# Optimization experiments

Measured on AMD Instinct MI355X. Metric: run time of the kernel, lower is better.

## Reference

```python
import jax, jax.numpy as jnp
import numpy as np

B, NWORD, HID = 4, 24, 512


def setup_inputs() -> dict:
    key = jax.random.key(0)
    ks = jax.random.split(key, 7)
    H = HID
    scale_in = 1.0 / np.sqrt(H)
    return {
        "seqt": jax.random.normal(ks[0], (B, NWORD, 2 * H), dtype=jnp.float32),
        # ins_input_linearity: Linear(H -> 5H) with bias
        "Wi": jax.random.normal(ks[1], (5 * H, H), dtype=jnp.float32) * scale_in,
        "bi": jnp.zeros((5 * H,), dtype=jnp.float32),
        # ins_state_linearity: Linear(H -> 5H) with bias (bias init: forget slots = 1)
        "Ws": jax.random.normal(ks[2], (5 * H, H), dtype=jnp.float32) * scale_in,
        "bs": jnp.zeros((5 * H,), dtype=jnp.float32).at[H:2 * H].set(1.0),
        # ins_bilinearity: BilinearSimilarity(2H, 2H) -> scalar x^T W y
        "Wbil": jax.random.normal(ks[3], (2 * H, 2 * H), dtype=jnp.float32) * (1.0 / (2.0 * H)),
    }


def reference(seqt, Wi, bi, Ws, bs, Wbil):
    """Inside pass (do_inside) of DioLstm in training mode (soft_sum over splits).

    Chart cell (left, L) covers words [left, left+L]. Returns root v = concat(h, c).
    """
    Bn, n, twoH = seqt.shape
    H = twoH // 2
    # ins_bias buffer: ones on the two forget-gate slots [H:3H]
    ins_bias = jnp.zeros((5 * H,), dtype=seqt.dtype).at[H:3 * H].set(1.0)

    def single(seq):  # seq: [n, 2H]
        chartH = jnp.zeros((n, n, H), seq.dtype).at[:, 0].set(seq[:, :H])
        chartC = jnp.zeros((n, n, H), seq.dtype).at[:, 0].set(seq[:, H:])
        chartS = jnp.zeros((n, n), seq.dtype)  # leaf scores are 0
        for L in range(1, n):  # span length - 1 (static unroll over diagonals)
            P = n - L  # number of spans on this diagonal
            lefts = jnp.arange(P)[:, None]          # [P,1]
            ksplit = jnp.arange(L)[None, :]          # [1,L]
            # left child: (left, k); right child: (left+k+1, L-1-k)
            lH = chartH[lefts, ksplit]; lC = chartC[lefts, ksplit]; lS = chartS[lefts, ksplit]
            ridx = lefts + ksplit + 1
            rlen = jnp.broadcast_to(L - 1 - ksplit, ridx.shape)
            rH = chartH[ridx, rlen]; rC = chartC[ridx, rlen]; rS = chartS[ridx, rlen]
            lv = jnp.concatenate([lH, lC], axis=-1)  # [P,L,2H]
            rv = jnp.concatenate([rH, rC], axis=-1)
            # bilinear compatibility + child scores
            compat = jnp.einsum('pki,ij,pkj->pk', lv, Wbil, rv) + lS + rS  # [P,L]
            # projected_input + projected_state (sum once; gate slices of the sum)
            proj = (lH @ Wi.T + bi + ins_bias) + (rH @ Ws.T + bs)  # [P,L,5H]
            ig, lf, rf, g, og = jnp.split(proj, 5, axis=-1)
            ig = jax.nn.sigmoid(ig); lf = jax.nn.sigmoid(lf); rf = jax.nn.sigmoid(rf)
            g = jnp.tanh(g); og = jax.nn.sigmoid(og)
            mem = lf * lC + rf * rC + ig * g
            h = og * jnp.tanh(mem)  # [P,L,H]
            # soft_sum: torch.tensor(s_set) detaches scores -> stop_gradient on weights
            sw = jax.lax.stop_gradient(compat)
            w = jax.nn.softmax(sw, axis=-1)  # [P,L]
            Hnew = jnp.einsum('pk,pkh->ph', w, h)
            Cnew = jnp.einsum('pk,pkh->ph', w, mem)
            Snew = jnp.sum(w * sw, axis=-1)
            pidx = jnp.arange(P)
            chartH = chartH.at[pidx, L].set(Hnew)
            chartC = chartC.at[pidx, L].set(Cnew)
            chartS = chartS.at[pidx, L].set(Snew)
        # root cell v = concat(h, c)
        return jnp.concatenate([chartH[0, n - 1], chartC[0, n - 1]], axis=0)

    return jax.vmap(single)(seqt)  # [B, 2H]
```

## Files before the change

kernel.cpp:

```cpp
#include <hip/hip_runtime.h>
#include <math.h>

#define NB 4
#define NW 24
#define H 512
#define H2 1024
#define H5 2560
#define NCELL 300
#define NEED_BYTES ((size_t)72<<20)

static float* g_buf = nullptr;
__attribute__((constructor)) static void dio_alloc_ws(){
  (void)hipMalloc((void**)&g_buf, NEED_BYTES);
}

typedef __attribute__((ext_vector_type(8))) short bf16x8;
typedef __attribute__((ext_vector_type(4))) float f32x4;
typedef unsigned short ushort_t;

__device__ __forceinline__ int coff(int l){ return l*NW - (l*(l-1))/2; }
__device__ __forceinline__ float sigm(float x){ return 1.f/(1.f+__expf(-x)); }
__device__ __forceinline__ float ftanh(float x){ return 1.f - 2.f/(__expf(2.f*x)+1.f); }

__device__ __forceinline__ ushort_t f2b(float x){
  unsigned int u = __float_as_uint(x);
  u += 0x7FFF + ((u>>16)&1);
  return (ushort_t)(u>>16);
}
__device__ __forceinline__ float b2f(ushort_t h){
  return __uint_as_float(((unsigned int)h)<<16);
}
__device__ __forceinline__ void split_store(ushort_t* __restrict__ ph,
                                            ushort_t* __restrict__ pl,
                                            size_t idx, float x){
  ushort_t h = f2b(x);
  ph[idx] = h;
  pl[idx] = f2b(x - b2f(h));
}

__global__ void k_init(const float* __restrict__ seqt,
                       const float* __restrict__ Wi, const float* __restrict__ Ws,
                       const float* __restrict__ Wbil,
                       ushort_t* __restrict__ WiBh, ushort_t* __restrict__ WiBl,
                       ushort_t* __restrict__ WsBh, ushort_t* __restrict__ WsBl,
                       ushort_t* __restrict__ WbilTh, ushort_t* __restrict__ WbilTl,
                       float* __restrict__ cH, float* __restrict__ cC, float* __restrict__ cS,
                       ushort_t* __restrict__ cHbh, ushort_t* __restrict__ cHbl,
                       ushort_t* __restrict__ cCbh, ushort_t* __restrict__ cCbl){
  const int blk = blockIdx.x, t = threadIdx.x;
  if (blk < 10240){
    int i = blk*256 + t;
    const int n = H5*H;
    if (i < n) split_store(WiBh, WiBl, i, Wi[i]);
    else       split_store(WsBh, WsBl, i-n, Ws[i-n]);
  } else if (blk < 11264){
    __shared__ float tile[32][33];
    int tb = blk - 10240;
    int tr = (tb>>5)*32, tc = (tb&31)*32;
    int tx = t & 31, ty = t >> 5;
    #pragma unroll
    for (int i=0;i<32;i+=8)
      tile[ty+i][tx] = Wbil[(size_t)(tr+ty+i)*H2 + tc+tx];
    __syncthreads();
    #pragma unroll
    for (int i=0;i<32;i+=8)
      split_store(WbilTh, WbilTl, (size_t)(tc+ty+i)*H2 + tr+tx, tile[tx][ty+i]);
  } else {
    int tid = (blk-11264)*256 + t;
    if (tid < NB*NW*H){
      int b = tid/(NW*H); int r = tid%(NW*H); int i = r/H; int d = r%H;
      size_t idx = (size_t)(b*NCELL + i)*H + d;
      float hv = seqt[(size_t)(b*NW+i)*H2 + d];
      float cv = seqt[(size_t)(b*NW+i)*H2 + H + d];
      cH[idx]=hv; cC[idx]=cv;
      split_store(cHbh,cHbl,idx,hv);
      split_store(cCbh,cCbl,idx,cv);
      if (d==0) cS[b*NCELL+i] = 0.f;
    }
  }
}

__device__ __forceinline__ void mfma3(f32x4& acc, bf16x8 ah, bf16x8 al,
                                      bf16x8 bh, bf16x8 bl){
  acc = __builtin_amdgcn_mfma_f32_16x16x32_bf16(ah, bh, acc, 0,0,0);
  acc = __builtin_amdgcn_mfma_f32_16x16x32_bf16(ah, bl, acc, 0,0,0);
  acc = __builtin_amdgcn_mfma_f32_16x16x32_bf16(al, bh, acc, 0,0,0);
}

__global__ void __launch_bounds__(256)
k_projN(const ushort_t* __restrict__ WiBh, const ushort_t* __restrict__ WiBl,
        const ushort_t* __restrict__ WsBh, const ushort_t* __restrict__ WsBl,
        const ushort_t* __restrict__ WbilTh, const ushort_t* __restrict__ WbilTl,
        const float* __restrict__ bi, const float* __restrict__ bs,
        const ushort_t* __restrict__ cHbh, const ushort_t* __restrict__ cHbl,
        const ushort_t* __restrict__ cCbh, const ushort_t* __restrict__ cCbl,
        float* __restrict__ cPI, float* __restrict__ cPS, float* __restrict__ cU,
        int d, int P)
{
  __shared__ f32x4 red[4][64];
  const int t = threadIdx.x, wave = t>>6, lane = t&63;
  const int jt = blockIdx.x;
  const int m0 = blockIdx.y*16;
  const int Mtot = NB*P;
  const int nm = min(16, Mtot-m0);

  int kind, j0;
  if (jt < 160){ kind=0; j0 = jt*16; }
  else if (jt < 320){ kind=1; j0 = (jt-160)*16; }
  else { kind=2; j0 = (jt-320)*16; }

  const int r = lane & 15;
  const int q = lane >> 4;

  int mg = m0 + (r < nm ? r : 0);
  const size_t arow = (size_t)((mg/P)*NCELL + coff(d) + mg%P)*H;

  f32x4 acc = {0.f,0.f,0.f,0.f};

  if (kind < 2){
    const ushort_t* bh_ = (kind==0 ? WiBh : WsBh) + (size_t)(j0+r)*H;
    const ushort_t* bl_ = (kind==0 ? WiBl : WsBl) + (size_t)(j0+r)*H;
    const int ks = wave*128 + q*8;
    bf16x8 fah[4], fal[4], fbh[4], fbl[4];
    #pragma unroll
    for (int s=0;s<4;s++){
      const int ko = ks + s*32;
      fah[s] = *(const bf16x8*)(cHbh + arow + ko);
      fal[s] = *(const bf16x8*)(cHbl + arow + ko);
      fbh[s] = *(const bf16x8*)(bh_ + ko);
      fbl[s] = *(const bf16x8*)(bl_ + ko);
    }
    #pragma unroll
    for (int s=0;s<4;s++) mfma3(acc, fah[s], fal[s], fbh[s], fbl[s]);
  } else {
    const ushort_t* bh_ = WbilTh + (size_t)(j0+r)*H2;
    const ushort_t* bl_ = WbilTl + (size_t)(j0+r)*H2;
    const ushort_t* ah_ = (wave<2 ? cHbh : cCbh) + arow;
    const ushort_t* al_ = (wave<2 ? cHbl : cCbl) + arow;
    const int kg0 = wave*256;
    const int ka0 = kg0 & 511;
    #pragma unroll
    for (int gz=0; gz<2; gz++){
      bf16x8 fah[4], fal[4], fbh[4], fbl[4];
      #pragma unroll
      for (int s=0;s<4;s++){
        const int so = (gz*4+s)*32 + q*8;
        fah[s] = *(const bf16x8*)(ah_ + ka0 + so);
        fal[s] = *(const bf16x8*)(al_ + ka0 + so);
        fbh[s] = *(const bf16x8*)(bh_ + kg0 + so);
        fbl[s] = *(const bf16x8*)(bl_ + kg0 + so);
      }
      #pragma unroll
      for (int s=0;s<4;s++) mfma3(acc, fah[s], fal[s], fbh[s], fbl[s]);
    }
  }

  red[wave][lane] = acc;
  __syncthreads();
  if (wave == 0){
    f32x4 s0 = red[0][lane], s1 = red[1][lane], s2 = red[2][lane], s3 = red[3][lane];
    f32x4 tot = (s0+s1) + (s2+s3);
    const int jo = j0 + r;
    float bias = 0.f;
    if (kind==0) bias = bi[jo] + ((jo>=H && jo<3*H)?1.f:0.f);
    else if (kind==1) bias = bs[jo];
    #pragma unroll
    for (int reg=0; reg<4; reg++){
      const int m = q*4 + reg;
      if (m < nm){
        const int mg2 = m0 + m;
        const size_t cell = (size_t)((mg2/P)*NCELL + coff(d) + mg2%P);
        const float v = tot[reg];
        if (kind==0)      cPI[cell*H5 + jo] = v + bias;
        else if (kind==1) cPS[cell*H5 + jo] = v + bias;
        else              cU [cell*H2 + jo] = v;
      }
    }
  }
}

__global__ void __launch_bounds__(256)
k_combine2(const float* __restrict__ cPI, const float* __restrict__ cPS,
           const float* __restrict__ cU,
           float* __restrict__ cH, float* __restrict__ cC, float* __restrict__ cS,
           ushort_t* __restrict__ cHbh, ushort_t* __restrict__ cHbl,
           ushort_t* __restrict__ cCbh, ushort_t* __restrict__ cCbl,
           int L, int P){
  const int t = threadIdx.x;
  const int b = blockIdx.x / P;
  const int left = blockIdx.x % P;
  const int dg = blockIdx.y;
  __shared__ float compat_s[32];
  __shared__ float wts_s[32];
  __shared__ float S_s;
  __shared__ float partH[128];
  __shared__ float partC[128];
  const int lane = t & 63;
  const int wv = t >> 6;
  for (int k=wv; k<L; k+=4){
    int lc = b*NCELL + coff(k) + left;
    int rc = b*NCELL + coff(L-1-k) + left+k+1;
    const float2* U2l = (const float2*)(cU + (size_t)lc*H2);
    const float2* U2h = (const float2*)(cU + (size_t)lc*H2 + H);
    const float2* Hr2 = (const float2*)(cH + (size_t)rc*H);
    const float2* Cr2 = (const float2*)(cC + (size_t)rc*H);
    float p = 0.f;
    #pragma unroll
    for (int it=0; it<4; it++){
      int i = lane + it*64;
      float2 u0 = U2l[i], u1 = U2h[i], hh = Hr2[i], cc = Cr2[i];
      p += u0.x*hh.x + u0.y*hh.y + u1.x*cc.x + u1.y*cc.y;
    }
    #pragma unroll
    for (int off=32; off>0; off>>=1) p += __shfl_down(p, off);
    if (lane==0) compat_s[k] = p + cS[lc] + cS[rc];
  }
  __syncthreads();
  if (t==0){
    float mx = -1e30f;
    for (int k=0;k<L;k++) mx = fmaxf(mx, compat_s[k]);
    float den = 0.f;
    for (int k=0;k<L;k++){ float e = __expf(compat_s[k]-mx); wts_s[k]=e; den+=e; }
    float inv = 1.f/den, S = 0.f;
    for (int k=0;k<L;k++){ wts_s[k]*=inv; S += wts_s[k]*compat_s[k]; }
    S_s = S;
  }
  __syncthreads();
  const int dloc = t & 127;
  const int dim = dg*128 + dloc;
  const int kpar = t >> 7;
  float aH = 0.f, aC = 0.f;
  for (int k=kpar; k<L; k+=2){
    float wk = wts_s[k];
    int lc = b*NCELL + coff(k) + left;
    int rc = b*NCELL + coff(L-1-k) + left+k+1;
    const float* PI = cPI + (size_t)lc*H5;
    const float* PS = cPS + (size_t)rc*H5;
    float p0 = PI[dim]     + PS[dim];
    float p1 = PI[H+dim]   + PS[H+dim];
    float p2 = PI[2*H+dim] + PS[2*H+dim];
    float p3 = PI[3*H+dim] + PS[3*H+dim];
    float p4 = PI[4*H+dim] + PS[4*H+dim];
    float lcv = cC[(size_t)lc*H + dim];
    float rcv = cC[(size_t)rc*H + dim];
    float mem = sigm(p1)*lcv + sigm(p2)*rcv + sigm(p0)*ftanh(p3);
    float h = sigm(p4)*ftanh(mem);
    aH += wk*h; aC += wk*mem;
  }
  if (kpar==1){ partH[dloc]=aH; partC[dloc]=aC; }
  __syncthreads();
  if (kpar==0){
    aH += partH[dloc];
    aC += partC[dloc];
    size_t nc = (size_t)(b*NCELL + coff(L) + left);
    cH[nc*H + dim] = aH;
    cC[nc*H + dim] = aC;
    split_store(cHbh,cHbl, nc*H + dim, aH);
    split_store(cCbh,cCbl, nc*H + dim, aC);
    if (t==0 && dg==0) cS[nc] = S_s;
  }
}

__global__ void k_out(const float* __restrict__ cH, const float* __restrict__ cC,
                      float* __restrict__ out){
  int tid = blockIdx.x*256+threadIdx.x;
  if (tid >= NB*H2) return;
  int b = tid>>10, d = tid&1023;
  int cell = b*NCELL + 299;
  out[tid] = (d<H) ? cH[(size_t)cell*H + d] : cC[(size_t)cell*H + (d-H)];
}

extern "C" void kernel_launch(void* const* d_in, const int* in_sizes, int n_in,
                              void* d_out, int out_size, void* d_ws, size_t ws_size,
                              hipStream_t stream){
  const float* seqt = (const float*)d_in[0];
  const float* Wi   = (const float*)d_in[1];
  const float* bi   = (const float*)d_in[2];
  const float* Ws   = (const float*)d_in[3];
  const float* bs   = (const float*)d_in[4];
  const float* Wbil = (const float*)d_in[5];
  float* out = (float*)d_out;

  float* p = (ws_size >= NEED_BYTES && g_buf == nullptr) ? (float*)d_ws : g_buf;
  float* cH  = p; p += (size_t)NB*NCELL*H;
  float* cC  = p; p += (size_t)NB*NCELL*H;
  float* cS  = p; p += (size_t)NB*NCELL;
  float* cPI = p; p += (size_t)NB*NCELL*H5;
  float* cPS = p; p += (size_t)NB*NCELL*H5;
  float* cU  = p; p += (size_t)NB*NCELL*H2;
  ushort_t* u = (ushort_t*)p;
  ushort_t* WiBh   = u; u += (size_t)H5*H;
  ushort_t* WiBl   = u; u += (size_t)H5*H;
  ushort_t* WsBh   = u; u += (size_t)H5*H;
  ushort_t* WsBl   = u; u += (size_t)H5*H;
  ushort_t* WbilTh = u; u += (size_t)H2*H2;
  ushort_t* WbilTl = u; u += (size_t)H2*H2;
  ushort_t* cHbh   = u; u += (size_t)NB*NCELL*H;
  ushort_t* cHbl   = u; u += (size_t)NB*NCELL*H;
  ushort_t* cCbh   = u; u += (size_t)NB*NCELL*H;
  ushort_t* cCbl   = u; u += (size_t)NB*NCELL*H;

  k_init<<<11456, 256, 0, stream>>>(seqt, Wi, Ws, Wbil,
      WiBh, WiBl, WsBh, WsBl, WbilTh, WbilTl,
      cH, cC, cS, cHbh, cHbl, cCbh, cCbl);

  k_projN<<<dim3(384, (NB*NW+15)/16), 256, 0, stream>>>(
      WiBh, WiBl, WsBh, WsBl, WbilTh, WbilTl, bi, bs,
      cHbh, cHbl, cCbh, cCbl, cPI, cPS, cU, 0, NW);
  for (int L=1; L<NW; L++){
    int P = NW - L;
    k_combine2<<<dim3(NB*P, 4), 256, 0, stream>>>(cPI, cPS, cU, cH, cC, cS,
                                                  cHbh, cHbl, cCbh, cCbl, L, P);
    if (L < NW-1)
      k_projN<<<dim3(384, (NB*P+15)/16), 256, 0, stream>>>(
          WiBh, WiBl, WsBh, WsBl, WbilTh, WbilTl, bi, bs,
          cHbh, cHbl, cCbh, cCbl, cPI, cPS, cU, L, P);
  }
  k_out<<<16, 256, 0, stream>>>(cH, cC, out);
}
```

Baseline: 690.8 us.

## Precompute next-diagonal compat scores inside combine and split work finer

The combine kernel now computes, in extra blocks, the bilinear compatibility scores for the next diagonal that only depend on already finished cells, storing them in a double-buffered scratch array. On the following step only the two new split scores are computed and the rest are read back. Combine also splits the hidden dimension into 16 groups of 32 with 8-way split parallelism, and the projection kernel uses 8 waves with shorter K slices. This removes the serial compat dot products from the critical path and raises parallelism, in exchange for extra blocks, scratch memory and a larger reduction.

```diff
diff --git a/kernel.cpp b/kernel.cpp
--- a/kernel.cpp
+++ b/kernel.cpp
@@ -36,6 +36,30 @@
   ushort_t h = f2b(x);
   ph[idx] = h;
   pl[idx] = f2b(x - b2f(h));
+}
+
+__device__ __forceinline__ float compat_dot(const float* __restrict__ cU,
+                                            const float* __restrict__ cH,
+                                            const float* __restrict__ cC,
+                                            const float* __restrict__ cS,
+                                            int lc, int rc, int lane){
+  const float4* U4  = (const float4*)(cU + (size_t)lc*H2);
+  const float4* Hr4 = (const float4*)(cH + (size_t)rc*H);
+  const float4* Cr4 = (const float4*)(cC + (size_t)rc*H);
+  float p = 0.f;
+  #pragma unroll
+  for (int it=0; it<2; it++){
+    float4 u = U4[lane + 64*it], h = Hr4[lane + 64*it];
+    p += u.x*h.x + u.y*h.y + u.z*h.z + u.w*h.w;
+  }
+  #pragma unroll
+  for (int it=0; it<2; it++){
+    float4 u = U4[128 + lane + 64*it], c = Cr4[lane + 64*it];
+    p += u.x*c.x + u.y*c.y + u.z*c.z + u.w*c.w;
+  }
+  #pragma unroll
+  for (int off=32; off>0; off>>=1) p += __shfl_down(p, off);
+  return p + cS[lc] + cS[rc];
 }
 
 __global__ void k_init(const float* __restrict__ seqt,
@@ -87,7 +111,7 @@
   acc = __builtin_amdgcn_mfma_f32_16x16x32_bf16(al, bh, acc, 0,0,0);
 }
 
-__global__ void __launch_bounds__(256)
+__global__ void __launch_bounds__(512)
 k_projN(const ushort_t* __restrict__ WiBh, const ushort_t* __restrict__ WiBl,
         const ushort_t* __restrict__ WsBh, const ushort_t* __restrict__ WsBl,
         const ushort_t* __restrict__ WbilTh, const ushort_t* __restrict__ WbilTl,
@@ -97,7 +121,7 @@
         float* __restrict__ cPI, float* __restrict__ cPS, float* __restrict__ cU,
         int d, int P)
 {
-  __shared__ f32x4 red[4][64];
+  __shared__ f32x4 red[8][64];
   const int t = threadIdx.x, wave = t>>6, lane = t&63;
   const int jt = blockIdx.x;
   const int m0 = blockIdx.y*16;
@@ -120,10 +144,10 @@
   if (kind < 2){
     const ushort_t* bh_ = (kind==0 ? WiBh : WsBh) + (size_t)(j0+r)*H;
     const ushort_t* bl_ = (kind==0 ? WiBl : WsBl) + (size_t)(j0+r)*H;
-    const int ks = wave*128 + q*8;
-    bf16x8 fah[4], fal[4], fbh[4], fbl[4];
-    #pragma unroll
-    for (int s=0;s<4;s++){
+    const int ks = wave*64 + q*8;
+    bf16x8 fah[2], fal[2], fbh[2], fbl[2];
+    #pragma unroll
+    for (int s=0;s<2;s++){
       const int ko = ks + s*32;
       fah[s] = *(const bf16x8*)(cHbh + arow + ko);
       fal[s] = *(const bf16x8*)(cHbl + arow + ko);
@@ -131,35 +155,33 @@
       fbl[s] = *(const bf16x8*)(bl_ + ko);
     }
     #pragma unroll
-    for (int s=0;s<4;s++) mfma3(acc, fah[s], fal[s], fbh[s], fbl[s]);
+    for (int s=0;s<2;s++) mfma3(acc, fah[s], fal[s], fbh[s], fbl[s]);
   } else {
     const ushort_t* bh_ = WbilTh + (size_t)(j0+r)*H2;
     const ushort_t* bl_ = WbilTl + (size_t)(j0+r)*H2;
-    const ushort_t* ah_ = (wave<2 ? cHbh : cCbh) + arow;
-    const ushort_t* al_ = (wave<2 ? cHbl : cCbl) + arow;
-    const int kg0 = wave*256;
+    const ushort_t* ah_ = (wave<4 ? cHbh : cCbh) + arow;
+    const ushort_t* al_ = (wave<4 ? cHbl : cCbl) + arow;
+    const int kg0 = wave*128;
     const int ka0 = kg0 & 511;
-    #pragma unroll
-    for (int gz=0; gz<2; gz++){
-      bf16x8 fah[4], fal[4], fbh[4], fbl[4];
-      #pragma unroll
-      for (int s=0;s<4;s++){
-        const int so = (gz*4+s)*32 + q*8;
-        fah[s] = *(const bf16x8*)(ah_ + ka0 + so);
-        fal[s] = *(const bf16x8*)(al_ + ka0 + so);
-        fbh[s] = *(const bf16x8*)(bh_ + kg0 + so);
-        fbl[s] = *(const bf16x8*)(bl_ + kg0 + so);
-      }
-      #pragma unroll
-      for (int s=0;s<4;s++) mfma3(acc, fah[s], fal[s], fbh[s], fbl[s]);
-    }
+    bf16x8 fah[4], fal[4], fbh[4], fbl[4];
+    #pragma unroll
+    for (int s=0;s<4;s++){
+      const int so = s*32 + q*8;
+      fah[s] = *(const bf16x8*)(ah_ + ka0 + so);
+      fal[s] = *(const bf16x8*)(al_ + ka0 + so);
+      fbh[s] = *(const bf16x8*)(bh_ + kg0 + so);
+      fbl[s] = *(const bf16x8*)(bl_ + kg0 + so);
+    }
+    #pragma unroll
+    for (int s=0;s<4;s++) mfma3(acc, fah[s], fal[s], fbh[s], fbl[s]);
   }
 
   red[wave][lane] = acc;
   __syncthreads();
   if (wave == 0){
-    f32x4 s0 = red[0][lane], s1 = red[1][lane], s2 = red[2][lane], s3 = red[3][lane];
-    f32x4 tot = (s0+s1) + (s2+s3);
+    f32x4 s0=red[0][lane], s1=red[1][lane], s2=red[2][lane], s3=red[3][lane];
+    f32x4 s4=red[4][lane], s5=red[5][lane], s6=red[6][lane], s7=red[7][lane];
+    f32x4 tot = ((s0+s1)+(s2+s3)) + ((s4+s5)+(s6+s7));
     const int jo = j0 + r;
     float bias = 0.f;
     if (kind==0) bias = bi[jo] + ((jo>=H && jo<3*H)?1.f:0.f);
@@ -180,41 +202,57 @@
 }
 
 __global__ void __launch_bounds__(256)
-k_combine2(const float* __restrict__ cPI, const float* __restrict__ cPS,
+k_combine3(const float* __restrict__ cPI, const float* __restrict__ cPS,
            const float* __restrict__ cU,
            float* __restrict__ cH, float* __restrict__ cC, float* __restrict__ cS,
            ushort_t* __restrict__ cHbh, ushort_t* __restrict__ cHbl,
            ushort_t* __restrict__ cCbh, ushort_t* __restrict__ cCbl,
+           const float* __restrict__ compatR, float* __restrict__ compatW,
            int L, int P){
   const int t = threadIdx.x;
-  const int b = blockIdx.x / P;
-  const int left = blockIdx.x % P;
-  const int dg = blockIdx.y;
+  const int lane = t & 63;
+  const int wave = t >> 6;
+  const int nphase = NB*P*16;
+  const int blk = blockIdx.x;
+
+  if (blk >= nphase){
+    const int P1 = P-1;
+    const int nterm = L-1;
+    int tid = (blk-nphase)*4 + wave;
+    if (P1 > 0 && nterm > 0 && tid < NB*P1*nterm){
+      int cell1 = tid / nterm;
+      int k = 1 + tid % nterm;
+      int b = cell1 / P1, left = cell1 % P1;
+      int lc = b*NCELL + coff(k) + left;
+      int rc = b*NCELL + coff(L-k) + left+k+1;
+      float v = compat_dot(cU, cH, cC, cS, lc, rc, lane);
+      if (lane==0) compatW[(b*NW + left)*NW + k] = v;
+    }
+    return;
+  }
+
+  const int cellid = blk >> 4;
+  const int dg = blk & 15;
+  const int b = cellid / P;
+  const int left = cellid % P;
   __shared__ float compat_s[32];
   __shared__ float wts_s[32];
   __shared__ float S_s;
-  __shared__ float partH[128];
-  __shared__ float partC[128];
-  const int lane = t & 63;
-  const int wv = t >> 6;
-  for (int k=wv; k<L; k+=4){
-    int lc = b*NCELL + coff(k) + left;
-    int rc = b*NCELL + coff(L-1-k) + left+k+1;
-    const float2* U2l = (const float2*)(cU + (size_t)lc*H2);
-    const float2* U2h = (const float2*)(cU + (size_t)lc*H2 + H);
-    const float2* Hr2 = (const float2*)(cH + (size_t)rc*H);
-    const float2* Cr2 = (const float2*)(cC + (size_t)rc*H);
-    float p = 0.f;
-    #pragma unroll
-    for (int it=0; it<4; it++){
-      int i = lane + it*64;
-      float2 u0 = U2l[i], u1 = U2h[i], hh = Hr2[i], cc = Cr2[i];
-      p += u0.x*hh.x + u0.y*hh.y + u1.x*cc.x + u1.y*cc.y;
-    }
-    #pragma unroll
-    for (int off=32; off>0; off>>=1) p += __shfl_down(p, off);
-    if (lane==0) compat_s[k] = p + cS[lc] + cS[rc];
-  }
+  __shared__ float partH[8][32];
+  __shared__ float partC[8][32];
+
+  if (wave == 0){
+    int lc = b*NCELL + left;
+    int rc = b*NCELL + coff(L-1) + left+1;
+    float v = compat_dot(cU, cH, cC, cS, lc, rc, lane);
+    if (lane==0) compat_s[0] = v;
+  } else if (wave == 1 && L >= 2){
+    int lc = b*NCELL + coff(L-1) + left;
+    int rc = b*NCELL + left+L;
+    float v = compat_dot(cU, cH, cC, cS, lc, rc, lane);
+    if (lane==0) compat_s[L-1] = v;
+  }
+  if (t >= 1 && t <= L-2) compat_s[t] = compatR[(b*NW + left)*NW + t];
   __syncthreads();
   if (t==0){
     float mx = -1e30f;
@@ -226,11 +264,11 @@
     S_s = S;
   }
   __syncthreads();
-  const int dloc = t & 127;
-  const int dim = dg*128 + dloc;
-  const int kpar = t >> 7;
+  const int dloc = t & 31;
+  const int dim = dg*32 + dloc;
+  const int kpar = t >> 5;
   float aH = 0.f, aC = 0.f;
-  for (int k=kpar; k<L; k+=2){
+  for (int k=kpar; k<L; k+=8){
     float wk = wts_s[k];
     int lc = b*NCELL + coff(k) + left;
     int rc = b*NCELL + coff(L-1-k) + left+k+1;
@@ -247,11 +285,11 @@
     float h = sigm(p4)*ftanh(mem);
     aH += wk*h; aC += wk*mem;
   }
-  if (kpar==1){ partH[dloc]=aH; partC[dloc]=aC; }
+  if (kpar > 0){ partH[kpar][dloc]=aH; partC[kpar][dloc]=aC; }
   __syncthreads();
-  if (kpar==0){
-    aH += partH[dloc];
-    aC += partC[dloc];
+  if (kpar == 0){
+    #pragma unroll
+    for (int q=1;q<8;q++){ aH += partH[q][dloc]; aC += partC[q][dloc]; }
     size_t nc = (size_t)(b*NCELL + coff(L) + left);
     cH[nc*H + dim] = aH;
     cC[nc*H + dim] = aC;
@@ -288,6 +326,8 @@
   float* cPI = p; p += (size_t)NB*NCELL*H5;
   float* cPS = p; p += (size_t)NB*NCELL*H5;
   float* cU  = p; p += (size_t)NB*NCELL*H2;
+  float* compatA = p; p += (size_t)NB*NW*NW;
+  float* compatB = p; p += (size_t)NB*NW*NW;
   ushort_t* u = (ushort_t*)p;
   ushort_t* WiBh   = u; u += (size_t)H5*H;
   ushort_t* WiBl   = u; u += (size_t)H5*H;
@@ -304,15 +344,20 @@
       WiBh, WiBl, WsBh, WsBl, WbilTh, WbilTl,
       cH, cC, cS, cHbh, cHbl, cCbh, cCbl);
 
-  k_projN<<<dim3(384, (NB*NW+15)/16), 256, 0, stream>>>(
+  k_projN<<<dim3(384, (NB*NW+15)/16), 512, 0, stream>>>(
       WiBh, WiBl, WsBh, WsBl, WbilTh, WbilTl, bi, bs,
       cHbh, cHbl, cCbh, cCbl, cPI, cPS, cU, 0, NW);
   for (int L=1; L<NW; L++){
     int P = NW - L;
-    k_combine2<<<dim3(NB*P, 4), 256, 0, stream>>>(cPI, cPS, cU, cH, cC, cS,
-                                                  cHbh, cHbl, cCbh, cCbl, L, P);
+    int P1 = P-1, nterm = L-1;
+    int wblk = (P1>0 && nterm>0) ? (NB*P1*nterm + 3)/4 : 0;
+    float* bufR = (L&1) ? compatA : compatB;
+    float* bufW = (L&1) ? compatB : compatA;
+    k_combine3<<<NB*P*16 + wblk, 256, 0, stream>>>(
+        cPI, cPS, cU, cH, cC, cS, cHbh, cHbl, cCbh, cCbl,
+        bufR, bufW, L, P);
     if (L < NW-1)
-      k_projN<<<dim3(384, (NB*P+15)/16), 256, 0, stream>>>(
+      k_projN<<<dim3(384, (NB*P+15)/16), 512, 0, stream>>>(
           WiBh, WiBl, WsBh, WsBl, WbilTh, WbilTl, bi, bs,
           cHbh, cHbl, cCbh, cCbl, cPI, cPS, cU, L, P);
   }
```

After: 625.9 us. -9.4%, faster.
